# Kernel optimization log

Hardware: AMD Instinct MI355X
Metric: run time of the kernel (lower is better)

The kernel has to match this reference:

```python
import jax, jax.numpy as jnp
import numpy as np

VOCAB = 50000
E = 256      # text_embed_dim
K = 512      # num_kernels
KS = 9       # kernel_size
L = 8192     # num labels
B, T = 8, 2048
PAD = KS // 2


def setup_inputs() -> dict:
    key = jax.random.key(0)
    ks = jax.random.split(key, 9)
    ids = jax.random.randint(ks[0], (B, T), 0, VOCAB)
    mask = jnp.ones((B, T), dtype=jnp.int32)  # unused by forward, kept for signature parity
    target = (jax.random.uniform(ks[1], (B, L)) < 0.01).astype(jnp.float32)
    embed_w = jax.random.normal(ks[2], (VOCAB, E), jnp.float32) * 0.02
    conv_w = jax.random.normal(ks[3], (K, E, KS), jnp.float32) * (1.0 / np.sqrt(E * KS))
    conv_b = jnp.zeros((K,), jnp.float32)
    U_w = jax.random.normal(ks[4], (L, K), jnp.float32) * (1.0 / np.sqrt(K))
    final_w = jax.random.normal(ks[5], (L, K), jnp.float32) * (1.0 / np.sqrt(K))
    final_b = jnp.zeros((L,), jnp.float32)
    return {"ids": ids, "mask": mask, "G": 0, "target": target,
            "embed_w": embed_w, "conv_w": conv_w, "conv_b": conv_b,
            "U_w": U_w, "final_w": final_w, "final_b": final_b}


def _forward(ids, embed_w, conv_w, conv_b, U_w, final_w, final_b):
    # embed + (dropout=identity in eval) -> [B, E, T]
    x = embed_w[ids].transpose(0, 2, 1)
    # same-padded Conv1d, then ReLU -> text_feats [B, T, K]
    y = jax.lax.conv_general_dilated(x, conv_w, (1,), [(PAD, PAD)],
                                     dimension_numbers=("NCH", "OIH", "NCH"))
    feats = jax.nn.relu(y + conv_b[None, :, None]).transpose(0, 2, 1)
    # label-wise attention: alpha = softmax(U.weight @ feats^T, dim=2) -> [B, L, T]
    scores = jnp.einsum("lk,btk->blt", U_w, feats)
    alpha = jax.nn.softmax(scores, axis=2)
    # attended features per label -> [B, L, K]
    attn = jnp.einsum("blt,btk->blk", alpha, feats)
    # label-wise dot with final.weight + bias -> logits [B, L]
    yhat = jnp.einsum("blk,lk->bl", attn, final_w) + final_b
    return yhat


def _bce_with_logits(yhat, target):
    # mean over all elements, numerically stable
    return jnp.mean(jnp.maximum(yhat, 0) - yhat * target + jnp.log1p(jnp.exp(-jnp.abs(yhat))))


def reference(ids, mask, G, target, embed_w, conv_w, conv_b, U_w, final_w, final_b):
    yhat = _forward(ids, embed_w, conv_w, conv_b, U_w, final_w, final_b)
    loss = _bce_with_logits(yhat, target)
    return yhat, loss
```

## Files before the change

### kernel.cpp

```cpp
#include <hip/hip_runtime.h>
#include <hip/hip_bf16.h>
#include <cstdint>

#define B_ 8
#define T_ 2048
#define E_ 256
#define K_ 512
#define KS_ 9
#define L_ 8192
#define PAD_ 4
#define TP_ (T_ + 2 * PAD_)
#define KK_ (E_ * KS_)

#define FEAT_SCALE 64.0f
#define W_SCALE 16.0f
#define INV_SS 9.765625e-4f

typedef __bf16 bf16x8 __attribute__((ext_vector_type(8)));
typedef float f32x4 __attribute__((ext_vector_type(4)));
typedef float f32x16 __attribute__((ext_vector_type(16)));

__device__ __forceinline__ unsigned short f2bf(float f) {
  union { float f; unsigned int u; } a; a.f = f;
  unsigned int r = (a.u + 0x7FFFu + ((a.u >> 16) & 1u)) >> 16;
  return (unsigned short)r;
}

__device__ __forceinline__ unsigned char f2fp8(float v) {
  return (unsigned char)(__builtin_amdgcn_cvt_pk_fp8_f32(v, v, 0, false) & 0xFF);
}

__device__ __forceinline__ unsigned int pk4_fp8(float a, float b, float c, float d) {
  int v = __builtin_amdgcn_cvt_pk_fp8_f32(a, b, 0, false);
  v = __builtin_amdgcn_cvt_pk_fp8_f32(c, d, v, true);
  return (unsigned int)v;
}

__device__ __forceinline__ void gld_lds16(const void* g, void* l) {
  __builtin_amdgcn_global_load_lds(
      (const __attribute__((address_space(1))) unsigned int*)g,
      (__attribute__((address_space(3))) unsigned int*)l, 16, 0, 0);
}

__device__ __forceinline__ f32x4 mfma_bf16(bf16x8 a, bf16x8 b, f32x4 c) {
  return __builtin_amdgcn_mfma_f32_16x16x32_bf16(a, b, c, 0, 0, 0);
}

__device__ __forceinline__ f32x16 mfma32_fp8(long long a, long long b, f32x16 c) {
  return __builtin_amdgcn_mfma_f32_32x32x16_fp8_fp8(a, b, c, 0, 0, 0);
}

__device__ __forceinline__ int swz_off(int k, int row) {
  int ku = k >> 4;
  int slot = (((ku & 7) ^ ((row >> 1) & 7)) | (ku & 24));
  return slot * 16 + ((((k >> 3) ^ row) & 1) << 3) + (k & 7);
}

__global__ __launch_bounds__(256) void k_embed(const int* __restrict__ ids,
                                               const float* __restrict__ emb,
                                               unsigned short* __restrict__ xpad) {
  int gid = blockIdx.x * 256 + threadIdx.x;
  int row = gid >> 6;
  int e4 = (gid & 63) << 2;
  int b = row / TP_;
  int tp = row - b * TP_;
  float4 v = make_float4(0.f, 0.f, 0.f, 0.f);
  if (tp >= PAD_ && tp < T_ + PAD_) {
    int id = ids[b * T_ + tp - PAD_];
    v = *(const float4*)(emb + (size_t)id * E_ + e4);
  }
  ushort4 o;
  o.x = f2bf(v.x); o.y = f2bf(v.y); o.z = f2bf(v.z); o.w = f2bf(v.w);
  *(ushort4*)(xpad + (size_t)row * E_ + e4) = o;
}

__global__ __launch_bounds__(256) void k_wt(const float* __restrict__ conv_w,
                                            unsigned short* __restrict__ wt) {
  int kk = blockIdx.x * 256 + threadIdx.x;
  int k = blockIdx.y;
  int j = kk >> 8, e = kk & 255;
  wt[(size_t)k * KK_ + kk] = f2bf(conv_w[(k * E_ + e) * KS_ + j]);
}

__global__ __launch_bounds__(256) void k_cast(const float* __restrict__ U_w,
                                              const float* __restrict__ F_w,
                                              unsigned char* __restrict__ u8,
                                              unsigned char* __restrict__ f8) {
  int gid = blockIdx.x * 256 + threadIdx.x;
  const float* src = blockIdx.y ? F_w : U_w;
  unsigned char* dst = blockIdx.y ? f8 : u8;
  int l = gid >> 6;
  int k0 = (gid & 63) << 3;
  const float* s = src + (size_t)l * K_ + k0;
  float4 v0 = *(const float4*)(s);
  float4 v1 = *(const float4*)(s + 4);
  uint2 o;
  o.x = pk4_fp8(v0.x * W_SCALE, v0.y * W_SCALE, v0.z * W_SCALE, v0.w * W_SCALE);
  o.y = pk4_fp8(v1.x * W_SCALE, v1.y * W_SCALE, v1.z * W_SCALE, v1.w * W_SCALE);
  *(uint2*)(dst + (size_t)l * K_ + swz_off(k0, l)) = o;
}

__global__ __launch_bounds__(512, 4) void k_conv(const unsigned short* __restrict__ xpad,
                                                 const unsigned short* __restrict__ wt,
                                                 const float* __restrict__ conv_b,
                                                 unsigned char* __restrict__ feats) {
  __shared__ char At[2][16384];
  __shared__ char Bt[2][16384];
  const int tid = threadIdx.x;
  const int lane = tid & 63;
  const int q = lane >> 4, c = lane & 15;
  const int w = tid >> 6;
  const int wi = w >> 1, wj = w & 1;
  const int b = blockIdx.z;
  const int t0 = blockIdx.y * 128;
  const int n0 = blockIdx.x * 128;

  const char* xb = (const char*)(xpad + (size_t)b * TP_ * E_);
  const char* wb = (const char*)wt;

  const char* asrc[2]; const char* bsrc[2]; int ldso[2];
#pragma unroll
  for (int rnd = 0; rnd < 2; ++rnd) {
    int u = rnd * 512 + tid;
    int r = u >> 3;
    int j = (u & 7) ^ (r & 7);
    asrc[rnd] = xb + (size_t)(t0 + r) * 512 + j * 16;
    bsrc[rnd] = wb + (size_t)(n0 + r) * (KK_ * 2) + j * 16;
    ldso[rnd] = u * 16;
  }

  int offA[2][2], offB[4][2];
#pragma unroll
  for (int li = 0; li < 2; ++li) {
    int r = wi * 32 + li * 16 + c;
#pragma unroll
    for (int h = 0; h < 2; ++h) offA[li][h] = r * 128 + (((4 * h + q) ^ (r & 7)) << 4);
  }
#pragma unroll
  for (int ti = 0; ti < 4; ++ti) {
    int r = wj * 64 + ti * 16 + c;
#pragma unroll
    for (int h = 0; h < 2; ++h) offB[ti][h] = r * 128 + (((4 * h + q) ^ (r & 7)) << 4);
  }

  f32x4 acc[2][4];
  f32x4 zero = {0.f, 0.f, 0.f, 0.f};
#pragma unroll
  for (int i = 0; i < 2; ++i)
#pragma unroll
    for (int j = 0; j < 4; ++j) acc[i][j] = zero;

#pragma unroll
  for (int rnd = 0; rnd < 2; ++rnd) {
    gld_lds16(asrc[rnd], At[0] + ldso[rnd]);
    gld_lds16(bsrc[rnd], Bt[0] + ldso[rnd]);
  }

  for (int it = 0; it < 36; ++it) {
    const int bsel = it & 1;
    __syncthreads();
    if (it != 35) {
      const int kkc = (it + 1) * 64;
      const int aofs = (kkc >> 8) * 512 + (kkc & 255) * 2;
      const int bofs = kkc * 2;
#pragma unroll
      for (int rnd = 0; rnd < 2; ++rnd) {
        gld_lds16(asrc[rnd] + aofs, At[bsel ^ 1] + ldso[rnd]);
        gld_lds16(bsrc[rnd] + bofs, Bt[bsel ^ 1] + ldso[rnd]);
      }
    }
    const char* aB = At[bsel];
    const char* bB = Bt[bsel];
#pragma unroll
    for (int h = 0; h < 2; ++h) {
      bf16x8 afr[2], bfr[4];
#pragma unroll
      for (int li = 0; li < 2; ++li) afr[li] = *(const bf16x8*)(aB + offA[li][h]);
#pragma unroll
      for (int ti = 0; ti < 4; ++ti) bfr[ti] = *(const bf16x8*)(bB + offB[ti][h]);
#pragma unroll
      for (int ti = 0; ti < 4; ++ti)
#pragma unroll
        for (int li = 0; li < 2; ++li)
          acc[li][ti] = mfma_bf16(afr[li], bfr[ti], acc[li][ti]);
    }
  }

#pragma unroll
  for (int ti = 0; ti < 4; ++ti) {
    int k = n0 + wj * 64 + ti * 16 + c;
    float bias = conv_b[k];
#pragma unroll
    for (int li = 0; li < 2; ++li) {
      int tb = t0 + wi * 32 + li * 16 + q * 4;
#pragma unroll
      for (int rr = 0; rr < 4; ++rr) {
        float v = fmaxf(acc[li][ti][rr] + bias, 0.f) * FEAT_SCALE;
        int t = tb + rr;
        feats[(size_t)(b * T_ + t) * K_ + swz_off(k, t)] = f2fp8(v);
      }
    }
  }
}

__global__ __launch_bounds__(512, 2) void k_attn(const unsigned char* __restrict__ feats,
                                                 const unsigned char* __restrict__ u8,
                                                 const unsigned char* __restrict__ f8,
                                                 const float* __restrict__ final_b,
                                                 float* __restrict__ out) {
  __shared__ char smem[131072];
  __shared__ float red[512];
  const int tid = threadIdx.x;
  const int lane = tid & 63;
  const int q2 = lane >> 5, c32 = lane & 31;
  const int w = tid >> 6;
  const int wi = w >> 1;
  const int wj = w & 1;
  const int b = blockIdx.y;
  const int l0 = blockIdx.x * 128;

  const unsigned char* fb = feats + (size_t)b * T_ * K_;

  char* Us = smem;
  char* Ws = smem + 65536;
#pragma unroll
  for (int rr = 0; rr < 8; ++rr) {
    gld_lds16(u8 + (size_t)l0 * K_ + rr * 8192 + tid * 16, Us + rr * 8192 + tid * 16);
    gld_lds16(f8 + (size_t)l0 * K_ + rr * 8192 + tid * 16, Ws + rr * 8192 + tid * 16);
  }
  __syncthreads();

  const int arow = wi * 32 + c32;
  const int ab = arow * 512 + (((q2 ^ arow) & 1) << 3);
  const int a3 = (arow >> 1) & 7;
  long long uf[32], wf[32];
#pragma unroll
  for (int s = 0; s < 32; ++s) {
    int off = ab + ((((s & 7) ^ a3) | (s & 24)) << 4);
    uf[s] = *(const long long*)(Us + off);
    wf[s] = *(const long long*)(Ws + off);
  }
  __syncthreads();

  char* const Fs0 = smem;
  char* const Fs1 = smem + 32768;
  const unsigned char* fsrc = fb + tid * 16;
#pragma unroll
  for (int rr = 0; rr < 4; ++rr)
    gld_lds16(fsrc + rr * 8192, Fs0 + tid * 16 + rr * 8192);

  const int brow = wj * 32 + c32;
  const int bb = brow * 512 + (((q2 ^ brow) & 1) << 3);
  const int b3 = (brow >> 1) & 7;

  f32x16 accS, accV;
  float num[16], den[16];
#pragma unroll
  for (int r = 0; r < 16; ++r) { accS[r] = 0.f; accV[r] = 0.f; num[r] = 0.f; den[r] = 0.f; }

  for (int tc = 0; tc < 32; ++tc) {
    const int bsel = tc & 1;
    char* const cur = bsel ? Fs1 : Fs0;
    char* const nxt = bsel ? Fs0 : Fs1;
    __syncthreads();
    if (tc != 31) {
      const unsigned char* nsrc = fsrc + (tc + 1) * 32768;
#pragma unroll
      for (int rr = 0; rr < 4; ++rr)
        gld_lds16(nsrc + rr * 8192, nxt + tid * 16 + rr * 8192);
    }
#pragma unroll
    for (int s = 0; s < 32; ++s) {
      long long fa = *(const long long*)(cur + bb + ((((s & 7) ^ b3) | (s & 24)) << 4));
      accS = mfma32_fp8(uf[s], fa, accS);
      accV = mfma32_fp8(wf[s], fa, accV);
    }
#pragma unroll
    for (int r = 0; r < 16; ++r) {
      float p = __expf(accS[r] * INV_SS);
      den[r] += p;
      num[r] += p * (accV[r] * INV_SS);
      accS[r] = 0.f;
      accV[r] = 0.f;
    }
  }

#pragma unroll
  for (int r = 0; r < 16; ++r) {
#pragma unroll
    for (int m = 1; m < 32; m <<= 1) {
      num[r] += __shfl_xor(num[r], m, 64);
      den[r] += __shfl_xor(den[r], m, 64);
    }
  }
  if (c32 == 0) {
#pragma unroll
    for (int r = 0; r < 16; ++r) {
      int ll = wi * 32 + (r & 3) + 8 * (r >> 2) + 4 * q2;
      red[wj * 256 + ll] = num[r];
      red[wj * 256 + 128 + ll] = den[r];
    }
  }
  __syncthreads();
  if (tid < 128) {
    int l = l0 + tid;
    float n = red[tid] + red[256 + tid];
    float d = red[128 + tid] + red[384 + tid];
    out[(size_t)b * L_ + l] = n / d + final_b[l];
  }
}

__global__ __launch_bounds__(256) void k_loss(const float* __restrict__ yhat,
                                              const float* __restrict__ target,
                                              float* __restrict__ loss) {
  int gid = blockIdx.x * 256 + threadIdx.x;
  float s = 0.f;
  for (int i = gid; i < B_ * L_; i += 64 * 256) {
    float y = yhat[i], t = target[i];
    s += fmaxf(y, 0.f) - y * t + log1pf(__expf(-fabsf(y)));
  }
#pragma unroll
  for (int m = 1; m < 64; m <<= 1) s += __shfl_xor(s, m, 64);
  if ((threadIdx.x & 63) == 0) atomicAdd(loss, s * (1.0f / (B_ * L_)));
}

extern "C" void kernel_launch(void* const* d_in, const int* in_sizes, int n_in,
                              void* d_out, int out_size, void* d_ws, size_t ws_size,
                              hipStream_t stream) {
  const int* ids = (const int*)d_in[0];
  const float* target = (const float*)d_in[3];
  const float* emb = (const float*)d_in[4];
  const float* conv_w = (const float*)d_in[5];
  const float* conv_b = (const float*)d_in[6];
  const float* U_w = (const float*)d_in[7];
  const float* F_w = (const float*)d_in[8];
  const float* final_b = (const float*)d_in[9];
  float* out = (float*)d_out;

  char* ws = (char*)d_ws;
  unsigned short* xpad = (unsigned short*)ws;
  size_t off = (size_t)B_ * TP_ * E_ * 2;
  unsigned short* wt = (unsigned short*)(ws + off);
  off += (size_t)K_ * KK_ * 2;
  unsigned char* u8 = (unsigned char*)(ws + off);
  off += (size_t)L_ * K_;
  unsigned char* f8 = (unsigned char*)(ws + off);
  off += (size_t)L_ * K_;
  unsigned char* feats = (unsigned char*)(ws + off);
  off += (size_t)B_ * T_ * K_;
  if (ws_size < off) return;

  k_embed<<<dim3((B_ * TP_ * 64) / 256), 256, 0, stream>>>(ids, emb, xpad);
  k_wt<<<dim3(KK_ / 256, K_), 256, 0, stream>>>(conv_w, wt);
  k_cast<<<dim3((L_ * K_ / 8) / 256, 2), 256, 0, stream>>>(U_w, F_w, u8, f8);
  k_conv<<<dim3(K_ / 128, T_ / 128, B_), 512, 0, stream>>>(xpad, wt, conv_b, feats);
  k_attn<<<dim3(L_ / 128, B_), 512, 0, stream>>>(feats, u8, f8, final_b, out);
  hipMemsetAsync(out + B_ * L_, 0, sizeof(float), stream);
  k_loss<<<dim3(64), 256, 0, stream>>>(out, target, out + B_ * L_);
}
```

Baseline: 352.2 us.

## Switch attention kernel to 32x32x64 scaled FP8 MFMA with new swizzle layout

Replaces the 32x32x16 FP8 MFMA in the attention kernel with the MX-scaled 32x32x64 f8f6f4 instruction (unit scales). This cuts the MFMA instruction count per chunk by a factor of four and widens LDS reads to 16-byte vector loads. The feature swizzle is changed to 16-byte granules XOR'd by row so each lane reads two contiguous 16-byte pieces. The INV_SS scaling of the value accumulator moves out of the inner loop into the final division. The new layout must match the writer in the conv kernel, which uses the shared swz_off helper, and the operand k-ordering must stay consistent between A and B.

```diff
diff --git a/kernel.cpp b/kernel.cpp
--- a/kernel.cpp
+++ b/kernel.cpp
@@ -19,6 +19,8 @@
 typedef __bf16 bf16x8 __attribute__((ext_vector_type(8)));
 typedef float f32x4 __attribute__((ext_vector_type(4)));
 typedef float f32x16 __attribute__((ext_vector_type(16)));
+typedef int i32x4 __attribute__((ext_vector_type(4)));
+typedef int i32x8 __attribute__((ext_vector_type(8)));
 
 __device__ __forceinline__ unsigned short f2bf(float f) {
   union { float f; unsigned int u; } a; a.f = f;
@@ -46,14 +48,14 @@
   return __builtin_amdgcn_mfma_f32_16x16x32_bf16(a, b, c, 0, 0, 0);
 }
 
-__device__ __forceinline__ f32x16 mfma32_fp8(long long a, long long b, f32x16 c) {
-  return __builtin_amdgcn_mfma_f32_32x32x16_fp8_fp8(a, b, c, 0, 0, 0);
+__device__ __forceinline__ f32x16 mfma_sc64(i32x8 a, i32x8 b, f32x16 c) {
+  return __builtin_amdgcn_mfma_scale_f32_32x32x64_f8f6f4(a, b, c, 0, 0, 0, 127, 0, 127);
 }
 
 __device__ __forceinline__ int swz_off(int k, int row) {
   int ku = k >> 4;
-  int slot = (((ku & 7) ^ ((row >> 1) & 7)) | (ku & 24));
-  return slot * 16 + ((((k >> 3) ^ row) & 1) << 3) + (k & 7);
+  int slot = ((ku & 7) ^ (row & 7)) | (ku & 24);
+  return slot * 16 + (k & 15);
 }
 
 __global__ __launch_bounds__(256) void k_embed(const int* __restrict__ ids,
@@ -208,7 +210,7 @@
                                                  const unsigned char* __restrict__ f8,
                                                  const float* __restrict__ final_b,
                                                  float* __restrict__ out) {
-  __shared__ char smem[131072];
+  __shared__ __align__(16) char smem[131072];
   __shared__ float red[512];
   const int tid = threadIdx.x;
   const int lane = tid & 63;
@@ -231,14 +233,19 @@
   __syncthreads();
 
   const int arow = wi * 32 + c32;
-  const int ab = arow * 512 + (((q2 ^ arow) & 1) << 3);
-  const int a3 = (arow >> 1) & 7;
-  long long uf[32], wf[32];
-#pragma unroll
-  for (int s = 0; s < 32; ++s) {
-    int off = ab + ((((s & 7) ^ a3) | (s & 24)) << 4);
-    uf[s] = *(const long long*)(Us + off);
-    wf[s] = *(const long long*)(Ws + off);
+  const int ab = arow * 512;
+  const int a7 = arow & 7;
+  i32x8 uf[8], wf[8];
+#pragma unroll
+  for (int s = 0; s < 8; ++s) {
+    int u0 = s * 4 + q2 * 2;
+    int o0 = ab + ((((u0 & 7) ^ a7) | (u0 & 24)) << 4);
+    i32x4 ul = *(const i32x4*)(Us + o0);
+    i32x4 uh = *(const i32x4*)(Us + (o0 ^ 16));
+    i32x4 wl = *(const i32x4*)(Ws + o0);
+    i32x4 wh = *(const i32x4*)(Ws + (o0 ^ 16));
+    uf[s] = __builtin_shufflevector(ul, uh, 0, 1, 2, 3, 4, 5, 6, 7);
+    wf[s] = __builtin_shufflevector(wl, wh, 0, 1, 2, 3, 4, 5, 6, 7);
   }
   __syncthreads();
 
@@ -250,8 +257,14 @@
     gld_lds16(fsrc + rr * 8192, Fs0 + tid * 16 + rr * 8192);
 
   const int brow = wj * 32 + c32;
-  const int bb = brow * 512 + (((q2 ^ brow) & 1) << 3);
-  const int b3 = (brow >> 1) & 7;
+  const int bb = brow * 512;
+  const int b7 = brow & 7;
+  int foff[8];
+#pragma unroll
+  for (int s = 0; s < 8; ++s) {
+    int u0 = s * 4 + q2 * 2;
+    foff[s] = bb + ((((u0 & 7) ^ b7) | (u0 & 24)) << 4);
+  }
 
   f32x16 accS, accV;
   float num[16], den[16];
@@ -270,16 +283,18 @@
         gld_lds16(nsrc + rr * 8192, nxt + tid * 16 + rr * 8192);
     }
 #pragma unroll
-    for (int s = 0; s < 32; ++s) {
-      long long fa = *(const long long*)(cur + bb + ((((s & 7) ^ b3) | (s & 24)) << 4));
-      accS = mfma32_fp8(uf[s], fa, accS);
-      accV = mfma32_fp8(wf[s], fa, accV);
+    for (int s = 0; s < 8; ++s) {
+      i32x4 flo = *(const i32x4*)(cur + foff[s]);
+      i32x4 fhi = *(const i32x4*)(cur + (foff[s] ^ 16));
+      i32x8 fa = __builtin_shufflevector(flo, fhi, 0, 1, 2, 3, 4, 5, 6, 7);
+      accS = mfma_sc64(uf[s], fa, accS);
+      accV = mfma_sc64(wf[s], fa, accV);
     }
 #pragma unroll
     for (int r = 0; r < 16; ++r) {
       float p = __expf(accS[r] * INV_SS);
       den[r] += p;
-      num[r] += p * (accV[r] * INV_SS);
+      num[r] += p * accV[r];
       accS[r] = 0.f;
       accV[r] = 0.f;
     }
@@ -306,7 +321,7 @@
     int l = l0 + tid;
     float n = red[tid] + red[256 + tid];
     float d = red[128 + tid] + red[384 + tid];
-    out[(size_t)b * L_ + l] = n / d + final_b[l];
+    out[(size_t)b * L_ + l] = (n * INV_SS) / d + final_b[l];
   }
 }
 
```

Measured after the change: 288.0 us. 18.2% less time.
